# Kernel optimization log

Hardware: AMD Instinct MI355X
Metric: run time of the kernel (lower is better)

The kernel has to match this reference:

```python
import jax, jax.numpy as jnp
import numpy as np

EPS = 1e-5

def layernorm(x, g, b):
    mu = jnp.mean(x, axis=-1, keepdims=True)
    var = jnp.mean(jnp.square(x - mu), axis=-1, keepdims=True)
    return (x - mu) * jax.lax.rsqrt(var + EPS) * g + b

def setup_inputs() -> dict:
    key = jax.random.key(0)
    ks = jax.random.split(key, 12)
    B, T, C, H = 4, 2048, 1024, 8
    Dh = C // H          # 128
    Dff = 4 * C          # 4096
    s = 0.02
    return {
        "x":     jax.random.normal(ks[0], (B, T, C), jnp.float32),
        "wq":    jax.random.normal(ks[1], (H, C, Dh), jnp.float32) * s,
        "wk":    jax.random.normal(ks[2], (H, C, Dh), jnp.float32) * s,
        "wv":    jax.random.normal(ks[3], (H, C, Dh), jnp.float32) * s,
        "w1":    jax.random.normal(ks[4], (C, Dff), jnp.float32) * s,
        "b1":    jnp.zeros((Dff,), jnp.float32),
        "w2":    jax.random.normal(ks[5], (Dff, C), jnp.float32) * s,
        "b2":    jnp.zeros((C,), jnp.float32),
        "ln1_g": jnp.ones((C,), jnp.float32),
        "ln1_b": jnp.zeros((C,), jnp.float32),
        "ln2_g": jnp.ones((C,), jnp.float32),
        "ln2_b": jnp.zeros((C,), jnp.float32),
    }

def reference(x, wq, wk, wv, w1, b1, w2, b2, ln1_g, ln1_b, ln2_g, ln2_b):
    B, T, C = x.shape
    H, _, Dh = wq.shape
    # --- multi-head self-attention (pre-LN) ---
    h = layernorm(x, ln1_g, ln1_b)
    q = jnp.einsum("btc,hcd->bhtd", h, wq)
    k = jnp.einsum("btc,hcd->bhtd", h, wk)
    v = jnp.einsum("btc,hcd->bhtd", h, wv)
    # NOTE: original multiplies by sqrt(head_size) (not divide) -- kept faithful
    scores = jnp.einsum("bhtd,bhsd->bhts", q, k) * (Dh ** 0.5)
    attn = jax.nn.softmax(scores, axis=-1)
    # dropout(p=0.2) treated as identity (eval mode)
    o = jnp.einsum("bhts,bhsd->bhtd", attn, v)
    # concat heads along last dim: head h fills contiguous slice
    o = o.transpose(0, 2, 1, 3).reshape(B, T, H * Dh)
    x = x + o  # no output projection in original module
    # --- feed-forward (pre-LN) ---
    h2 = layernorm(x, ln2_g, ln2_b)
    ff = jax.nn.relu(h2 @ w1 + b1) @ w2 + b2
    return x + ff
```

## Files before the change

kernel.cpp:

```cpp
#include <hip/hip_runtime.h>
#include <hip/hip_bf16.h>
#include <math.h>

#define B_   4
#define T_   2048
#define C_   1024
#define H_   8
#define DH   128
#define DFF  4096
#define M_   (B_*T_)

typedef __attribute__((ext_vector_type(8))) short bf16x8;
typedef __attribute__((ext_vector_type(4))) float f32x4;

#define SC2 16.32223094f

__device__ __forceinline__ unsigned short f2bf(float x) {
  union { float f; unsigned u; } v; v.f = x;
  return (unsigned short)((v.u + 0x7fffu + ((v.u >> 16) & 1u)) >> 16);
}
__device__ __forceinline__ float bf2f(unsigned short h) {
  union { unsigned u; float f; } v; v.u = ((unsigned)h) << 16; return v.f;
}

__device__ __forceinline__ f32x4 mfma_bf16(bf16x8 a, bf16x8 b, f32x4 c) {
  return __builtin_amdgcn_mfma_f32_16x16x32_bf16(a, b, c, 0, 0, 0);
}

__device__ __forceinline__ void gll16(const void* g, void* l) {
  __builtin_amdgcn_global_load_lds((const __attribute__((address_space(1))) void*)g,
                                   (__attribute__((address_space(3))) void*)l,
                                   16, 0, 0);
}

__global__ __launch_bounds__(256) void ln_kernel(const float* __restrict__ in,
                                                 const float* __restrict__ g,
                                                 const float* __restrict__ bb,
                                                 unsigned short* __restrict__ h_hi,
                                                 unsigned short* __restrict__ h_lo) {
  __shared__ float red[8];
  const int row = blockIdx.x;
  const int tid = threadIdx.x;
  const float* p = in + (size_t)row * C_;
  const float4 xv = *(const float4*)(p + (tid << 2));
  float s  = xv.x + xv.y + xv.z + xv.w;
  float sq = xv.x*xv.x + xv.y*xv.y + xv.z*xv.z + xv.w*xv.w;
  #pragma unroll
  for (int off = 32; off > 0; off >>= 1) {
    s  += __shfl_xor(s, off);
    sq += __shfl_xor(sq, off);
  }
  if ((tid & 63) == 0) { red[(tid >> 6) * 2] = s; red[(tid >> 6) * 2 + 1] = sq; }
  __syncthreads();
  s  = red[0] + red[2] + red[4] + red[6];
  sq = red[1] + red[3] + red[5] + red[7];
  const float mu  = s * (1.0f / C_);
  const float var = sq * (1.0f / C_) - mu * mu;
  const float rs  = rsqrtf(var + 1e-5f);
  const float4 gv = *(const float4*)(g  + (tid << 2));
  const float4 bv = *(const float4*)(bb + (tid << 2));
  float ov[4];
  ov[0] = (xv.x - mu) * rs * gv.x + bv.x;
  ov[1] = (xv.y - mu) * rs * gv.y + bv.y;
  ov[2] = (xv.z - mu) * rs * gv.z + bv.z;
  ov[3] = (xv.w - mu) * rs * gv.w + bv.w;
  ushort4 hv, lv;
  unsigned short* hp = (unsigned short*)&hv;
  unsigned short* lp = (unsigned short*)&lv;
  #pragma unroll
  for (int j = 0; j < 4; ++j) {
    hp[j] = f2bf(ov[j]);
    lp[j] = f2bf(ov[j] - bf2f(hp[j]));
  }
  *(ushort4*)(h_hi + (size_t)row * C_ + (tid << 2)) = hv;
  *(ushort4*)(h_lo + (size_t)row * C_ + (tid << 2)) = lv;
}

__global__ __launch_bounds__(256) void cvt_t_kernel(const float* __restrict__ in,
                                                    unsigned short* __restrict__ out,
                                                    int R, int CC) {
  __shared__ float tile[32][33];
  const int r0 = blockIdx.y << 5, c0 = blockIdx.x << 5;
  const int tr = threadIdx.x >> 3, tc4 = (threadIdx.x & 7) << 2;
  const float4 vv = *(const float4*)(in + (size_t)(r0 + tr) * CC + c0 + tc4);
  tile[tr][tc4+0] = vv.x; tile[tr][tc4+1] = vv.y;
  tile[tr][tc4+2] = vv.z; tile[tr][tc4+3] = vv.w;
  __syncthreads();
  ushort4 o;
  o.x = f2bf(tile[tc4+0][tr]); o.y = f2bf(tile[tc4+1][tr]);
  o.z = f2bf(tile[tc4+2][tr]); o.w = f2bf(tile[tc4+3][tr]);
  *(ushort4*)(out + (size_t)(c0 + tr) * R + r0 + tc4) = o;
}

__global__ __launch_bounds__(256) void cvt_qkv_kernel(const float* __restrict__ wq,
                                                      const float* __restrict__ wk,
                                                      const float* __restrict__ wv,
                                                      unsigned short* __restrict__ wt_hi,
                                                      unsigned short* __restrict__ wt_lo) {
  const int z = blockIdx.z;
  const int which = z >> 3, head = z & 7;
  const float* in = (which == 0 ? wq : (which == 1 ? wk : wv)) + (size_t)head * C_ * DH;
  unsigned short* oh = wt_hi + (size_t)z * DH * C_;
  unsigned short* ol = wt_lo + (size_t)z * DH * C_;
  __shared__ float tile[32][33];
  const int r0 = blockIdx.y << 5, c0 = blockIdx.x << 5;
  const int tr = threadIdx.x >> 3, tc4 = (threadIdx.x & 7) << 2;
  const float4 vv = *(const float4*)(in + (size_t)(r0 + tr) * DH + c0 + tc4);
  tile[tr][tc4+0] = vv.x; tile[tr][tc4+1] = vv.y;
  tile[tr][tc4+2] = vv.z; tile[tr][tc4+3] = vv.w;
  __syncthreads();
  ushort4 hv, lv;
  unsigned short* hp = (unsigned short*)&hv;
  unsigned short* lp = (unsigned short*)&lv;
  #pragma unroll
  for (int j = 0; j < 4; ++j) {
    const float val = tile[tc4+j][tr];
    hp[j] = f2bf(val);
    lp[j] = f2bf(val - bf2f(hp[j]));
  }
  *(ushort4*)(oh + (size_t)(c0 + tr) * C_ + r0 + tc4) = hv;
  *(ushort4*)(ol + (size_t)(c0 + tr) * C_ + r0 + tc4) = lv;
}

template<int TERMS>
__device__ __forceinline__ void gemm128_mfma(
    const unsigned short* __restrict__ Ah, const unsigned short* __restrict__ Al,
    int lda,
    const unsigned short* __restrict__ Bh, const unsigned short* __restrict__ Bl,
    int ldb, int K, f32x4 (&acc)[4][4],
    unsigned short* AhS, unsigned short* AlS,
    unsigned short* BhS, unsigned short* BlS) {
  const int tid  = threadIdx.x;
  const int w    = tid >> 6;
  const int lane = tid & 63;
  const int l15  = lane & 15, quad = lane >> 4;
  const int srow = lane >> 2, skc = (lane & 3) << 3;
  const int wm = w & 1, wn = w >> 1;

  for (int k0 = 0; k0 < K; k0 += 32) {
    __syncthreads();
    #pragma unroll
    for (int i = 0; i < 2; ++i) {
      const int seg  = w * 2 + i;
      const int r    = seg * 16 + srow;
      const int lofs = seg * 512 + lane * 8;
      gll16(Ah + (size_t)r * lda + k0 + skc, AhS + lofs);
      gll16(Bh + (size_t)r * ldb + k0 + skc, BhS + lofs);
      if (TERMS == 3) {
        gll16(Al + (size_t)r * lda + k0 + skc, AlS + lofs);
        gll16(Bl + (size_t)r * ldb + k0 + skc, BlS + lofs);
      }
    }
    __syncthreads();
    bf16x8 aH[4], bH[4], aL[4], bL[4];
    #pragma unroll
    for (int t = 0; t < 4; ++t) {
      aH[t] = *(const bf16x8*)&AhS[(wm * 64 + t * 16 + l15) * 32 + quad * 8];
      bH[t] = *(const bf16x8*)&BhS[(wn * 64 + t * 16 + l15) * 32 + quad * 8];
      if (TERMS == 3) {
        aL[t] = *(const bf16x8*)&AlS[(wm * 64 + t * 16 + l15) * 32 + quad * 8];
        bL[t] = *(const bf16x8*)&BlS[(wn * 64 + t * 16 + l15) * 32 + quad * 8];
      }
    }
    #pragma unroll
    for (int rt = 0; rt < 4; ++rt)
      #pragma unroll
      for (int ct = 0; ct < 4; ++ct) {
        if (TERMS == 3) {
          acc[rt][ct] = mfma_bf16(aL[rt], bH[ct], acc[rt][ct]);
          acc[rt][ct] = mfma_bf16(aH[rt], bL[ct], acc[rt][ct]);
        }
        acc[rt][ct] = mfma_bf16(aH[rt], bH[ct], acc[rt][ct]);
      }
  }
}

__global__ __launch_bounds__(256) void qkm_kernel(const unsigned short* __restrict__ h_hi,
                                                  const unsigned short* __restrict__ h_lo,
                                                  const unsigned short* __restrict__ wt_hi,
                                                  const unsigned short* __restrict__ wt_lo,
                                                  unsigned short* __restrict__ q_hi,
                                                  unsigned short* __restrict__ q_lo,
                                                  unsigned short* __restrict__ k_hi,
                                                  unsigned short* __restrict__ k_lo) {
  __shared__ __align__(16) unsigned short AhS[4096], AlS[4096];
  __shared__ __align__(16) unsigned short BhS[4096], BlS[4096];
  const int m0 = blockIdx.x << 7;
  const int z  = blockIdx.y;
  const int which = z >> 3, head = z & 7;
  f32x4 acc[4][4];
  #pragma unroll
  for (int i = 0; i < 4; ++i)
    #pragma unroll
    for (int j = 0; j < 4; ++j)
      #pragma unroll
      for (int r = 0; r < 4; ++r) acc[i][j][r] = 0.f;
  gemm128_mfma<3>(h_hi + (size_t)m0 * C_, h_lo + (size_t)m0 * C_, C_,
                  wt_hi + (size_t)z * DH * C_, wt_lo + (size_t)z * DH * C_, C_,
                  C_, acc, AhS, AlS, BhS, BlS);
  const int lane = threadIdx.x & 63, w = threadIdx.x >> 6;
  const int l15 = lane & 15, quad = lane >> 4;
  const int wm = w & 1, wn = w >> 1;
  const int bh = (m0 >> 11) * H_ + head;
  const int tbase = (m0 & (T_ - 1)) + wm * 64 + quad * 4;
  if (which == 0) {
    #pragma unroll
    for (int rt = 0; rt < 4; ++rt)
      #pragma unroll
      for (int ct = 0; ct < 4; ++ct) {
        const int d = wn * 64 + ct * 16 + l15;
        #pragma unroll
        for (int r = 0; r < 4; ++r) {
          const int t = tbase + rt * 16 + r;
          const float val = acc[rt][ct][r] * SC2;
          const unsigned short hb = f2bf(val);
          const size_t idx = ((size_t)bh * T_ + t) * DH + d;
          q_hi[idx] = hb;
          q_lo[idx] = f2bf(val - bf2f(hb));
        }
      }
  } else {
    #pragma unroll
    for (int rt = 0; rt < 4; ++rt)
      #pragma unroll
      for (int ct = 0; ct < 4; ++ct) {
        const int d = wn * 64 + ct * 16 + l15;
        #pragma unroll
        for (int r = 0; r < 4; ++r) {
          const int t = tbase + rt * 16 + r;
          const float val = acc[rt][ct][r];
          const unsigned short hb = f2bf(val);
          const size_t idx = (((size_t)bh * 64 + (t >> 5)) * 4 + (d >> 5)) * 1024
                           + (size_t)(t & 31) * 32 + (d & 31);
          k_hi[idx] = hb;
          k_lo[idx] = f2bf(val - bf2f(hb));
        }
      }
  }
}

__global__ __launch_bounds__(256) void vm_kernel(const unsigned short* __restrict__ h_hi,
                                                 const unsigned short* __restrict__ wv_hi,
                                                 unsigned short* __restrict__ vimg) {
  __shared__ __align__(16) unsigned short AhS[4096], BhS[4096];
  const int m0 = blockIdx.x << 7;
  const int head = blockIdx.y;
  f32x4 acc[4][4];
  #pragma unroll
  for (int i = 0; i < 4; ++i)
    #pragma unroll
    for (int j = 0; j < 4; ++j)
      #pragma unroll
      for (int r = 0; r < 4; ++r) acc[i][j][r] = 0.f;
  gemm128_mfma<1>(h_hi + (size_t)m0 * C_, nullptr, C_,
                  wv_hi + (size_t)(16 + head) * DH * C_, nullptr, C_,
                  C_, acc, AhS, nullptr, BhS, nullptr);
  const int lane = threadIdx.x & 63, w = threadIdx.x >> 6;
  const int l15 = lane & 15, quad = lane >> 4;
  const int wm = w & 1, wn = w >> 1;
  const int bh = (m0 >> 11) * H_ + head;
  #pragma unroll
  for (int rt = 0; rt < 4; ++rt)
    #pragma unroll
    for (int ct = 0; ct < 4; ++ct) {
      const int d  = wn * 64 + ct * 16 + l15;
      const int t0 = (m0 & (T_ - 1)) + wm * 64 + rt * 16 + quad * 4;
      ushort4 pk;
      pk.x = f2bf(acc[rt][ct][0]); pk.y = f2bf(acc[rt][ct][1]);
      pk.z = f2bf(acc[rt][ct][2]); pk.w = f2bf(acc[rt][ct][3]);
      *(ushort4*)&vimg[(((size_t)bh * 64 + (t0 >> 5)) * 128 + d) * 32 + (t0 & 31)] = pk;
    }
}

__global__ __launch_bounds__(256) void ff1_kernel(const unsigned short* __restrict__ h2,
                                                  const unsigned short* __restrict__ w1t,
                                                  const float* __restrict__ b1,
                                                  unsigned short* __restrict__ ff1) {
  __shared__ __align__(16) unsigned short AhS[4096], BhS[4096];
  const int n0 = blockIdx.x << 7;
  const int m0 = blockIdx.y << 7;
  f32x4 acc[4][4];
  #pragma unroll
  for (int i = 0; i < 4; ++i)
    #pragma unroll
    for (int j = 0; j < 4; ++j)
      #pragma unroll
      for (int r = 0; r < 4; ++r) acc[i][j][r] = 0.f;
  gemm128_mfma<1>(h2 + (size_t)m0 * C_, nullptr, C_,
                  w1t + (size_t)n0 * C_, nullptr, C_,
                  C_, acc, AhS, nullptr, BhS, nullptr);
  const int lane = threadIdx.x & 63, w = threadIdx.x >> 6;
  const int l15 = lane & 15, quad = lane >> 4;
  const int wm = w & 1, wn = w >> 1;
  #pragma unroll
  for (int rt = 0; rt < 4; ++rt)
    #pragma unroll
    for (int ct = 0; ct < 4; ++ct) {
      const int n = n0 + wn * 64 + ct * 16 + l15;
      const float bias = b1[n];
      #pragma unroll
      for (int r = 0; r < 4; ++r) {
        const int m = m0 + wm * 64 + rt * 16 + quad * 4 + r;
        ff1[(size_t)m * DFF + n] = f2bf(fmaxf(acc[rt][ct][r] + bias, 0.f));
      }
    }
}

__global__ __launch_bounds__(256) void ff2_kernel(const unsigned short* __restrict__ ff1,
                                                  const unsigned short* __restrict__ w2t,
                                                  const float* __restrict__ b2,
                                                  const float* __restrict__ xo,
                                                  float* __restrict__ out) {
  __shared__ __align__(16) unsigned short AhS[4096], BhS[4096];
  const int n0 = blockIdx.x << 7;
  const int m0 = blockIdx.y << 7;
  f32x4 acc[4][4];
  #pragma unroll
  for (int i = 0; i < 4; ++i)
    #pragma unroll
    for (int j = 0; j < 4; ++j)
      #pragma unroll
      for (int r = 0; r < 4; ++r) acc[i][j][r] = 0.f;
  gemm128_mfma<1>(ff1 + (size_t)m0 * DFF, nullptr, DFF,
                  w2t + (size_t)n0 * DFF, nullptr, DFF,
                  DFF, acc, AhS, nullptr, BhS, nullptr);
  const int lane = threadIdx.x & 63, w = threadIdx.x >> 6;
  const int l15 = lane & 15, quad = lane >> 4;
  const int wm = w & 1, wn = w >> 1;
  #pragma unroll
  for (int rt = 0; rt < 4; ++rt)
    #pragma unroll
    for (int ct = 0; ct < 4; ++ct) {
      const int n = n0 + wn * 64 + ct * 16 + l15;
      const float bias = b2[n];
      #pragma unroll
      for (int r = 0; r < 4; ++r) {
        const int m = m0 + wm * 64 + rt * 16 + quad * 4 + r;
        out[(size_t)m * C_ + n] = acc[rt][ct][r] + bias + xo[(size_t)m * C_ + n];
      }
    }
}

#define BQ 128

__global__ __launch_bounds__(256, 2) void attn_kernel(
    const unsigned short* __restrict__ q_hi, const unsigned short* __restrict__ q_lo,
    const unsigned short* __restrict__ k_hi, const unsigned short* __restrict__ k_lo,
    const unsigned short* __restrict__ vimg,
    const float* __restrict__ x, float* __restrict__ xo) {
  __shared__ __align__(16) unsigned short KhS[4096];
  __shared__ __align__(16) unsigned short KlS[4096];
  __shared__ __align__(16) unsigned short VtS[4096];
  __shared__ __align__(16) unsigned short PS [4096];

  const int bh  = blockIdx.y;
  const int qt0 = blockIdx.x * BQ;
  const int tid  = threadIdx.x;
  const int w    = tid >> 6;
  const int lane = tid & 63;
  const int l15  = lane & 15;
  const int quad = lane >> 4;

  bf16x8 Qh[2][4], Ql[2][4];
  #pragma unroll
  for (int rt = 0; rt < 2; ++rt) {
    const int row = qt0 + w * 32 + rt * 16 + l15;
    #pragma unroll
    for (int kc = 0; kc < 4; ++kc) {
      const size_t off = ((size_t)bh * T_ + row) * DH + kc * 32 + quad * 8;
      Qh[rt][kc] = *(const bf16x8*)(q_hi + off);
      Ql[rt][kc] = *(const bf16x8*)(q_lo + off);
    }
  }

  f32x4 O[2][8];
  #pragma unroll
  for (int rt = 0; rt < 2; ++rt)
    #pragma unroll
    for (int n = 0; n < 8; ++n)
      #pragma unroll
      for (int r = 0; r < 4; ++r) O[rt][n][r] = 0.f;
  float m_i[2][4], l_i[2][4];
  #pragma unroll
  for (int rt = 0; rt < 2; ++rt)
    #pragma unroll
    for (int r = 0; r < 4; ++r) { m_i[rt][r] = -1e30f; l_i[rt][r] = 0.f; }

  for (int kt = 0; kt < T_ / 32; ++kt) {
    const size_t tb = ((size_t)bh * 64 + kt) * 4096;
    __syncthreads();
    #pragma unroll
    for (int i = 0; i < 2; ++i) {
      const int ofs = (w * 2 + i) * 512 + lane * 8;
      gll16(k_hi + tb + ofs, KhS + ofs);
      gll16(k_lo + tb + ofs, KlS + ofs);
      gll16(vimg + tb + ofs, VtS + ofs);
    }
    __syncthreads();

    f32x4 S[2][2];
    #pragma unroll
    for (int rt = 0; rt < 2; ++rt)
      #pragma unroll
      for (int ct = 0; ct < 2; ++ct)
        #pragma unroll
        for (int r = 0; r < 4; ++r) S[rt][ct][r] = 0.f;
    #pragma unroll
    for (int kc = 0; kc < 4; ++kc) {
      const int o = kc * 1024 + quad * 8;
      const bf16x8 bh0 = *(const bf16x8*)&KhS[o + l15 * 32];
      const bf16x8 bh1 = *(const bf16x8*)&KhS[o + (16 + l15) * 32];
      const bf16x8 bl0 = *(const bf16x8*)&KlS[o + l15 * 32];
      const bf16x8 bl1 = *(const bf16x8*)&KlS[o + (16 + l15) * 32];
      #pragma unroll
      for (int rt = 0; rt < 2; ++rt) {
        S[rt][0] = mfma_bf16(Ql[rt][kc], bh0, S[rt][0]);
        S[rt][0] = mfma_bf16(Qh[rt][kc], bl0, S[rt][0]);
        S[rt][0] = mfma_bf16(Qh[rt][kc], bh0, S[rt][0]);
        S[rt][1] = mfma_bf16(Ql[rt][kc], bh1, S[rt][1]);
        S[rt][1] = mfma_bf16(Qh[rt][kc], bl1, S[rt][1]);
        S[rt][1] = mfma_bf16(Qh[rt][kc], bh1, S[rt][1]);
      }
    }

    #pragma unroll
    for (int rt = 0; rt < 2; ++rt) {
      #pragma unroll
      for (int r = 0; r < 4; ++r) {
        const float s0 = S[rt][0][r];
        const float s1 = S[rt][1][r];
        float mx = fmaxf(s0, s1);
        #pragma unroll
        for (int msk = 1; msk < 16; msk <<= 1) mx = fmaxf(mx, __shfl_xor(mx, msk));
        const float m_new = fmaxf(m_i[rt][r], mx);
        const float alpha = exp2f(m_i[rt][r] - m_new);
        m_i[rt][r] = m_new;
        const float p0 = exp2f(s0 - m_new);
        const float p1 = exp2f(s1 - m_new);
        float rs = p0 + p1;
        #pragma unroll
        for (int msk = 1; msk < 16; msk <<= 1) rs += __shfl_xor(rs, msk);
        l_i[rt][r] = l_i[rt][r] * alpha + rs;
        #pragma unroll
        for (int n = 0; n < 8; ++n) O[rt][n][r] *= alpha;
        const int prow = w * 32 + rt * 16 + quad * 4 + r;
        PS[prow * 32 + l15]      = (unsigned short)(__float_as_uint(p0) >> 16);
        PS[prow * 32 + 16 + l15] = (unsigned short)(__float_as_uint(p1) >> 16);
      }
    }
    __syncthreads();

    bf16x8 aP[2];
    #pragma unroll
    for (int rt = 0; rt < 2; ++rt)
      aP[rt] = *(const bf16x8*)&PS[(w * 32 + rt * 16 + l15) * 32 + quad * 8];
    #pragma unroll
    for (int n = 0; n < 8; ++n) {
      const bf16x8 bv = *(const bf16x8*)&VtS[(n * 16 + l15) * 32 + quad * 8];
      O[0][n] = mfma_bf16(aP[0], bv, O[0][n]);
      O[1][n] = mfma_bf16(aP[1], bv, O[1][n]);
    }
  }

  const int b = bh >> 3, hh = bh & 7;
  #pragma unroll
  for (int rt = 0; rt < 2; ++rt) {
    #pragma unroll
    for (int r = 0; r < 4; ++r) {
      const float inv_l = 1.0f / l_i[rt][r];
      const int t = qt0 + w * 32 + rt * 16 + quad * 4 + r;
      const size_t xrow = ((size_t)(b * T_ + t)) * C_ + (size_t)hh * DH;
      #pragma unroll
      for (int n = 0; n < 8; ++n) {
        const int d = n * 16 + l15;
        xo[xrow + d] = x[xrow + d] + O[rt][n][r] * inv_l;
      }
    }
  }
}

extern "C" void kernel_launch(void* const* d_in, const int* in_sizes, int n_in,
                              void* d_out, int out_size, void* d_ws, size_t ws_size,
                              hipStream_t stream) {
  (void)in_sizes; (void)n_in; (void)out_size; (void)ws_size;
  const float* x     = (const float*)d_in[0];
  const float* wq    = (const float*)d_in[1];
  const float* wk    = (const float*)d_in[2];
  const float* wv    = (const float*)d_in[3];
  const float* w1    = (const float*)d_in[4];
  const float* b1    = (const float*)d_in[5];
  const float* w2    = (const float*)d_in[6];
  const float* b2    = (const float*)d_in[7];
  const float* ln1_g = (const float*)d_in[8];
  const float* ln1_b = (const float*)d_in[9];
  const float* ln2_g = (const float*)d_in[10];
  const float* ln2_b = (const float*)d_in[11];
  float* out = (float*)d_out;

  char* W = (char*)d_ws;
  float* xo = (float*)(W);
  unsigned short* q_hi  = (unsigned short*)(W + (32u  << 20));
  unsigned short* q_lo  = (unsigned short*)(W + (48u  << 20));
  unsigned short* k_hi  = (unsigned short*)(W + (64u  << 20));
  unsigned short* k_lo  = (unsigned short*)(W + (80u  << 20));
  unsigned short* vimg  = (unsigned short*)(W + (96u  << 20));
  unsigned short* ff1   = (unsigned short*)(W + (32u  << 20));
  unsigned short* h_hi  = (unsigned short*)(W + (112u << 20));
  unsigned short* h_lo  = (unsigned short*)(W + (128u << 20));
  unsigned short* w1t   = (unsigned short*)(W + (144u << 20));
  unsigned short* w2t   = (unsigned short*)(W + (152u << 20));
  unsigned short* wt_hi = (unsigned short*)(W + (160u << 20));
  unsigned short* wt_lo = (unsigned short*)(W + (166u << 20));

  cvt_t_kernel<<<dim3(DFF / 32, C_ / 32), 256, 0, stream>>>(w1, w1t, C_, DFF);
  cvt_t_kernel<<<dim3(C_ / 32, DFF / 32), 256, 0, stream>>>(w2, w2t, DFF, C_);
  cvt_qkv_kernel<<<dim3(DH / 32, C_ / 32, 24), 256, 0, stream>>>(wq, wk, wv, wt_hi, wt_lo);
  ln_kernel<<<M_, 256, 0, stream>>>(x, ln1_g, ln1_b, h_hi, h_lo);
  qkm_kernel<<<dim3(M_ / 128, 16), 256, 0, stream>>>(h_hi, h_lo, wt_hi, wt_lo,
                                                     q_hi, q_lo, k_hi, k_lo);
  vm_kernel<<<dim3(M_ / 128, H_), 256, 0, stream>>>(h_hi, wt_hi, vimg);
  attn_kernel<<<dim3(T_ / BQ, B_ * H_), 256, 0, stream>>>(q_hi, q_lo, k_hi, k_lo,
                                                          vimg, x, xo);
  ln_kernel<<<M_, 256, 0, stream>>>(xo, ln2_g, ln2_b, h_hi, h_lo);
  ff1_kernel<<<dim3(DFF / 128, M_ / 128), 256, 0, stream>>>(h_hi, w1t, b1, ff1);
  ff2_kernel<<<dim3(C_ / 128, M_ / 128), 256, 0, stream>>>(ff1, w2t, b2, xo, out);
}
```

Before: 714.7 us.

## Split attention over key dimension into two parts with combine kernel

New measurement: 1.012 ms. +41.6%, slower.

```diff
diff --git a/kernel.cpp b/kernel.cpp
--- a/kernel.cpp
+++ b/kernel.cpp
@@ -343,18 +343,20 @@
 
 #define BQ 128
 
-__global__ __launch_bounds__(256, 2) void attn_kernel(
+__global__ __launch_bounds__(256, 4) void attn_kernel(
     const unsigned short* __restrict__ q_hi, const unsigned short* __restrict__ q_lo,
     const unsigned short* __restrict__ k_hi, const unsigned short* __restrict__ k_lo,
     const unsigned short* __restrict__ vimg,
-    const float* __restrict__ x, float* __restrict__ xo) {
+    unsigned short* __restrict__ Opart,
+    float* __restrict__ mP, float* __restrict__ lP) {
   __shared__ __align__(16) unsigned short KhS[4096];
   __shared__ __align__(16) unsigned short KlS[4096];
   __shared__ __align__(16) unsigned short VtS[4096];
   __shared__ __align__(16) unsigned short PS [4096];
 
-  const int bh  = blockIdx.y;
-  const int qt0 = blockIdx.x * BQ;
+  const int bh   = blockIdx.y;
+  const int qt0  = blockIdx.x * BQ;
+  const int part = blockIdx.z;
   const int tid  = threadIdx.x;
   const int w    = tid >> 6;
   const int lane = tid & 63;
@@ -386,7 +388,7 @@
     #pragma unroll
     for (int r = 0; r < 4; ++r) { m_i[rt][r] = -1e30f; l_i[rt][r] = 0.f; }
 
-  for (int kt = 0; kt < T_ / 32; ++kt) {
+  for (int kt = part * 32; kt < part * 32 + 32; ++kt) {
     const size_t tb = ((size_t)bh * 64 + kt) * 4096;
     __syncthreads();
     #pragma unroll
@@ -462,21 +464,46 @@
     }
   }
 
+  unsigned short* Ob = Opart + ((size_t)(part * 32 + bh)) * T_ * DH;
+  float* mrow = mP + (size_t)(part * 32 + bh) * T_;
+  float* lrow = lP + (size_t)(part * 32 + bh) * T_;
+  #pragma unroll
+  for (int rt = 0; rt < 2; ++rt) {
+    #pragma unroll
+    for (int r = 0; r < 4; ++r) {
+      const int t = qt0 + w * 32 + rt * 16 + quad * 4 + r;
+      if (l15 == 0) { mrow[t] = m_i[rt][r]; lrow[t] = l_i[rt][r]; }
+      #pragma unroll
+      for (int n = 0; n < 8; ++n)
+        Ob[(size_t)t * DH + n * 16 + l15] = f2bf(O[rt][n][r]);
+    }
+  }
+}
+
+__global__ __launch_bounds__(256) void comb_kernel(
+    const unsigned short* __restrict__ Opart,
+    const float* __restrict__ mP, const float* __restrict__ lP,
+    const float* __restrict__ x, float* __restrict__ xo) {
+  const int rid = blockIdx.x * 8 + (threadIdx.x >> 5);
+  const int d4  = (threadIdx.x & 31) << 2;
+  const int bh = rid >> 11, t = rid & (T_ - 1);
+  const float m0 = mP[rid], m1 = mP[rid + 32 * T_];
+  const float l0 = lP[rid], l1 = lP[rid + 32 * T_];
+  const float m  = fmaxf(m0, m1);
+  const float a0 = exp2f(m0 - m), a1 = exp2f(m1 - m);
+  const float inv = 1.0f / (l0 * a0 + l1 * a1);
+  const size_t o0 = (size_t)rid * DH + d4;
+  const ushort4 u0 = *(const ushort4*)(Opart + o0);
+  const ushort4 u1 = *(const ushort4*)(Opart + o0 + (size_t)32 * T_ * DH);
   const int b = bh >> 3, hh = bh & 7;
-  #pragma unroll
-  for (int rt = 0; rt < 2; ++rt) {
-    #pragma unroll
-    for (int r = 0; r < 4; ++r) {
-      const float inv_l = 1.0f / l_i[rt][r];
-      const int t = qt0 + w * 32 + rt * 16 + quad * 4 + r;
-      const size_t xrow = ((size_t)(b * T_ + t)) * C_ + (size_t)hh * DH;
-      #pragma unroll
-      for (int n = 0; n < 8; ++n) {
-        const int d = n * 16 + l15;
-        xo[xrow + d] = x[xrow + d] + O[rt][n][r] * inv_l;
-      }
-    }
-  }
+  const size_t xi = ((size_t)(b * T_ + t)) * C_ + hh * DH + d4;
+  const float4 xv = *(const float4*)(x + xi);
+  float4 ov;
+  ov.x = xv.x + (bf2f(u0.x) * a0 + bf2f(u1.x) * a1) * inv;
+  ov.y = xv.y + (bf2f(u0.y) * a0 + bf2f(u1.y) * a1) * inv;
+  ov.z = xv.z + (bf2f(u0.z) * a0 + bf2f(u1.z) * a1) * inv;
+  ov.w = xv.w + (bf2f(u0.w) * a0 + bf2f(u1.w) * a1) * inv;
+  *(float4*)(xo + xi) = ov;
 }
 
 extern "C" void kernel_launch(void* const* d_in, const int* in_sizes, int n_in,
@@ -507,10 +534,13 @@
   unsigned short* ff1   = (unsigned short*)(W + (32u  << 20));
   unsigned short* h_hi  = (unsigned short*)(W + (112u << 20));
   unsigned short* h_lo  = (unsigned short*)(W + (128u << 20));
+  unsigned short* Opart = (unsigned short*)(W + (112u << 20));
   unsigned short* w1t   = (unsigned short*)(W + (144u << 20));
   unsigned short* w2t   = (unsigned short*)(W + (152u << 20));
   unsigned short* wt_hi = (unsigned short*)(W + (160u << 20));
   unsigned short* wt_lo = (unsigned short*)(W + (166u << 20));
+  float*          mPf   = (float*)(W + (172u << 20));
+  float*          lPf   = (float*)(W + (173u << 20));
 
   cvt_t_kernel<<<dim3(DFF / 32, C_ / 32), 256, 0, stream>>>(w1, w1t, C_, DFF);
   cvt_t_kernel<<<dim3(C_ / 32, DFF / 32), 256, 0, stream>>>(w2, w2t, DFF, C_);
@@ -519,8 +549,9 @@
   qkm_kernel<<<dim3(M_ / 128, 16), 256, 0, stream>>>(h_hi, h_lo, wt_hi, wt_lo,
                                                      q_hi, q_lo, k_hi, k_lo);
   vm_kernel<<<dim3(M_ / 128, H_), 256, 0, stream>>>(h_hi, wt_hi, vimg);
-  attn_kernel<<<dim3(T_ / BQ, B_ * H_), 256, 0, stream>>>(q_hi, q_lo, k_hi, k_lo,
-                                                          vimg, x, xo);
+  attn_kernel<<<dim3(T_ / BQ, B_ * H_, 2), 256, 0, stream>>>(q_hi, q_lo, k_hi, k_lo,
+                                                             vimg, Opart, mPf, lPf);
+  comb_kernel<<<(32 * T_) / 8, 256, 0, stream>>>(Opart, mPf, lPf, x, xo);
   ln_kernel<<<M_, 256, 0, stream>>>(xo, ln2_g, ln2_b, h_hi, h_lo);
   ff1_kernel<<<dim3(DFF / 128, M_ / 128), 256, 0, stream>>>(h_hi, w1t, b1, ff1);
   ff2_kernel<<<dim3(C_ / 128, M_ / 128), 256, 0, stream>>>(ff1, w2t, b2, xo, out);
```
